# Kernel optimization log

Hardware: AMD Instinct MI355X
Metric: run time of the kernel (lower is better)

The kernel has to match this reference:

```python
import jax, jax.numpy as jnp
import numpy as np

N = 100000
D = 128
E = 1600000
NUM_STEPS = 8
LAM0 = 1.0
LAM1 = 1.0
ALPHA = 1.0 / (1.0 + 0.0 + LAM0 + LAM1)  # args.alp == 0 path


def setup_inputs() -> dict:
    key = jax.random.key(0)
    ks = jax.random.split(key, 12)
    X = jax.random.normal(ks[0], (N, D), dtype=jnp.float32)
    # H init: normal(0, 1/in_features) + I  (notresidual=False branch)
    H1 = jax.random.normal(ks[1], (D, D), dtype=jnp.float32) * (1.0 / D) + jnp.eye(D, dtype=jnp.float32)
    H2 = jax.random.normal(ks[2], (D, D), dtype=jnp.float32) * (1.0 / D) + jnp.eye(D, dtype=jnp.float32)
    w_beta = jax.random.uniform(ks[3], (E,), dtype=jnp.float32)
    w_gamma = jax.random.uniform(ks[4], (E,), dtype=jnp.float32)
    d_beta = jax.random.uniform(ks[5], (N,), dtype=jnp.float32)
    d_gamma = jax.random.uniform(ks[6], (N,), dtype=jnp.float32)
    src_beta = jax.random.randint(ks[7], (E,), 0, N, dtype=jnp.int32)
    dst_beta = jax.random.randint(ks[8], (E,), 0, N, dtype=jnp.int32)
    src_gamma = jax.random.randint(ks[9], (E,), 0, N, dtype=jnp.int32)
    dst_gamma = jax.random.randint(ks[10], (E,), 0, N, dtype=jnp.int32)
    return {"X": X, "H1": H1, "H2": H2, "w_beta": w_beta, "w_gamma": w_gamma,
            "d_beta": d_beta, "d_gamma": d_gamma,
            "src_beta": src_beta, "dst_beta": dst_beta,
            "src_gamma": src_gamma, "dst_gamma": dst_gamma}


def _spmm(w, src, dst, Y):
    # (sparse A) @ Y with A[dst, src] = w
    return jax.ops.segment_sum(w[:, None] * Y[src], dst, num_segments=N)


def reference(X, H1, H2, w_beta, w_gamma, d_beta, d_gamma,
              src_beta, dst_beta, src_gamma, dst_gamma):
    # Q_tild = lam0*D_beta + lam1*D_gamma + I  (diagonal)
    q = LAM0 * d_beta + LAM1 * d_gamma + 1.0  # [N]
    S1 = H1 + H1.T
    P1 = H1 @ H1.T
    S2 = H2 + H2.T
    P2 = H2 @ H2.T
    Y0 = X
    Y = X
    for _ in range(NUM_STEPS):
        AbY = _spmm(w_beta, src_beta, dst_beta, Y)    # A_beta @ Y
        AgY = _spmm(w_gamma, src_gamma, dst_gamma, Y)  # A_gamma @ Y
        term_beta = AbY @ S1 - d_beta[:, None] * (Y @ P1)
        # L_gamma @ Y = D_gamma@Y - A_gamma@Y
        term_gamma = (d_gamma[:, None] * Y - AgY
                      + AgY @ S2 - d_gamma[:, None] * (Y @ P2))
        Y_hat = LAM0 * term_beta + Y0 + LAM1 * term_gamma
        Y = (1.0 - ALPHA) * Y + ALPHA * (Y_hat / q[:, None])
    return Y
```

## Files before the change

kernel.cpp:

```cpp
#include <hip/hip_runtime.h>
#include <cstdint>
#include <cstddef>

#define DD 128
#define ATS 68
#define ARS 132
#define BQS 132


__global__ void count2_k(const int* __restrict__ dstb, const int* __restrict__ dstg,
                         int* __restrict__ degb, int* __restrict__ degg, int E, int gE) {
    int b = blockIdx.x;
    const int* dst = (b < gE) ? dstb : dstg;
    int* deg = (b < gE) ? degb : degg;
    int i = ((b < gE) ? b : b - gE) * blockDim.x + threadIdx.x;
    if (i < E) atomicAdd(&deg[dst[i]], 1);
}

__global__ __launch_bounds__(1024) void scan2_k(const int* __restrict__ degb,
                                                const int* __restrict__ degg,
                                                int* __restrict__ rpb, int* __restrict__ rpg,
                                                int* __restrict__ curb, int* __restrict__ curg,
                                                int n) {
    const int* deg = (blockIdx.x == 0) ? degb : degg;
    int* rp = (blockIdx.x == 0) ? rpb : rpg;
    int* cur = (blockIdx.x == 0) ? curb : curg;
    __shared__ int sums[1024];
    int tid = threadIdx.x;
    int per = (n + 1023) >> 10;
    int start = tid * per;
    int end = min(start + per, n);
    int s = 0;
    for (int i = start; i < end; ++i) s += deg[i];
    sums[tid] = s;
    __syncthreads();
    for (int off = 1; off < 1024; off <<= 1) {
        int v = (tid >= off) ? sums[tid - off] : 0;
        __syncthreads();
        sums[tid] += v;
        __syncthreads();
    }
    int pre = (tid == 0) ? 0 : sums[tid - 1];
    for (int i = start; i < end; ++i) {
        rp[i] = pre;
        cur[i] = pre;
        pre += deg[i];
    }
    if (end == n) rp[n] = pre;
}

__global__ void fill2_k(const int* __restrict__ srcb, const int* __restrict__ dstb,
                        const float* __restrict__ wb,
                        const int* __restrict__ srcg, const int* __restrict__ dstg,
                        const float* __restrict__ wg,
                        int* __restrict__ curb, int* __restrict__ curg,
                        int2* __restrict__ eb, int2* __restrict__ eg, int E, int gE) {
    int b = blockIdx.x;
    bool isb = (b < gE);
    const int* src = isb ? srcb : srcg;
    const int* dst = isb ? dstb : dstg;
    const float* w = isb ? wb : wg;
    int* cur = isb ? curb : curg;
    int2* edges = isb ? eb : eg;
    int i = (isb ? b : b - gE) * blockDim.x + threadIdx.x;
    if (i < E) {
        int d = dst[i];
        int pos = atomicAdd(&cur[d], 1);
        edges[pos] = make_int2(src[i], __float_as_int(w[i]));
    }
}


__global__ __launch_bounds__(256) void prep_k(const float* __restrict__ H,
                                              float* __restrict__ P,
                                              float* __restrict__ S) {
    int idx = blockIdx.x * 256 + threadIdx.x;
    int i = idx >> 7, j = idx & 127;
    float acc = 0.f;
    for (int k = 0; k < DD; ++k) acc += H[i * DD + k] * H[j * DD + k];
    P[idx] = acc;
    S[idx] = H[i * DD + j] + H[j * DD + i];
}


__global__ __launch_bounds__(256, 3) void step_k(
    const float* __restrict__ Yc, const float* __restrict__ X,
    const int* __restrict__ rpb, const int2* __restrict__ eb,
    const int* __restrict__ rpg, const int2* __restrict__ eg,
    const float* __restrict__ db, const float* __restrict__ dg,
    const float* __restrict__ P1, const float* __restrict__ P2,
    const float* __restrict__ S1, const float* __restrict__ S2,
    float* __restrict__ Yn, int n)
{
    __shared__ float At[DD * ATS];
    __shared__ float U[32 * ARS];

    const int tid = threadIdx.x;
    const int lane = tid & 63;
    const int wv = tid >> 6;
    const int cg = tid & 15;
    const int rg = tid >> 4;
    const int row0 = blockIdx.x * 64;

    float aS[4][8], aP1[4][8], aP2[4][8];
#pragma unroll
    for (int i = 0; i < 4; ++i)
#pragma unroll
        for (int j = 0; j < 8; ++j) { aS[i][j] = 0.f; aP1[i][j] = 0.f; aP2[i][j] = 0.f; }

    auto gatherA = [&](const int* __restrict__ rp, const int2* __restrict__ edges) {
        for (int h = 0; h < 2; ++h) {
#pragma unroll 1
            for (int it = 0; it < 8; ++it) {
                int r = wv * 8 + it;
                int node = row0 + h * 32 + r;
                float a0 = 0.f, a1 = 0.f;
                if (node < n) {
                    int beg = rp[node], end = rp[node + 1];
                    int j = beg;
                    for (; j + 4 <= end; j += 4) {
                        int2 e0 = edges[j + 0], e1 = edges[j + 1];
                        int2 e2 = edges[j + 2], e3 = edges[j + 3];
                        float2 f0 = *((const float2*)(Yc + (size_t)e0.x * DD) + lane);
                        float2 f1 = *((const float2*)(Yc + (size_t)e1.x * DD) + lane);
                        float2 f2 = *((const float2*)(Yc + (size_t)e2.x * DD) + lane);
                        float2 f3 = *((const float2*)(Yc + (size_t)e3.x * DD) + lane);
                        float w0 = __int_as_float(e0.y), w1 = __int_as_float(e1.y);
                        float w2 = __int_as_float(e2.y), w3 = __int_as_float(e3.y);
                        a0 += w0 * f0.x; a1 += w0 * f0.y;
                        a0 += w1 * f1.x; a1 += w1 * f1.y;
                        a0 += w2 * f2.x; a1 += w2 * f2.y;
                        a0 += w3 * f3.x; a1 += w3 * f3.y;
                    }
                    for (; j < end; ++j) {
                        int2 e = edges[j];
                        float2 f = *((const float2*)(Yc + (size_t)e.x * DD) + lane);
                        float wv2 = __int_as_float(e.y);
                        a0 += wv2 * f.x; a1 += wv2 * f.y;
                    }
                }
                *reinterpret_cast<float2*>(&U[r * ARS + 2 * lane]) = make_float2(a0, a1);
            }
            __syncthreads();
            {
                int r = tid & 31;
                int cb = (tid >> 5) * 16;
#pragma unroll
                for (int u = 0; u < 4; ++u) {
                    float4 v = *reinterpret_cast<const float4*>(&U[r * ARS + cb + 4 * u]);
                    int c = cb + 4 * u;
                    At[(c + 0) * ATS + h * 32 + r] = v.x;
                    At[(c + 1) * ATS + h * 32 + r] = v.y;
                    At[(c + 2) * ATS + h * 32 + r] = v.z;
                    At[(c + 3) * ATS + h * 32 + r] = v.w;
                }
            }
            __syncthreads();
        }
    };

    auto stageY = [&]() {
        int r = tid >> 2;
        int rowc = min(row0 + r, n - 1);
        const float* gp = Yc + (size_t)rowc * DD;
#pragma unroll
        for (int i = 0; i < 8; ++i) {
            int c = ((tid & 3) << 2) + (i << 4);
            float4 v = *reinterpret_cast<const float4*>(gp + c);
            At[(c + 0) * ATS + r] = v.x;
            At[(c + 1) * ATS + r] = v.y;
            At[(c + 2) * ATS + r] = v.z;
            At[(c + 3) * ATS + r] = v.w;
        }
    };

    auto gemm = [&](const float* __restrict__ M, float (&acc)[4][8]) {
#pragma unroll 1
        for (int kq = 0; kq < 4; ++kq) {
            {
                int kl = tid & 31;
                int cb = (tid >> 5) * 16;
                const float* gp = M + (size_t)(kq * 32 + kl) * DD + cb;
                float* bp = U + kl * BQS + cb;
#pragma unroll
                for (int u = 0; u < 4; ++u)
                    *reinterpret_cast<float4*>(bp + 4 * u) =
                        *reinterpret_cast<const float4*>(gp + 4 * u);
            }
            __syncthreads();
#pragma unroll 2
            for (int kl = 0; kl < 32; ++kl) {
                int k = kq * 32 + kl;
                float4 a = *reinterpret_cast<const float4*>(&At[k * ATS + rg * 4]);
                float4 b0 = *reinterpret_cast<const float4*>(&U[kl * BQS + cg * 4]);
                float4 b1 = *reinterpret_cast<const float4*>(&U[kl * BQS + 64 + cg * 4]);
                float av[4] = {a.x, a.y, a.z, a.w};
                float bv[8] = {b0.x, b0.y, b0.z, b0.w, b1.x, b1.y, b1.z, b1.w};
#pragma unroll
                for (int i = 0; i < 4; ++i)
#pragma unroll
                    for (int j = 0; j < 8; ++j) acc[i][j] += av[i] * bv[j];
            }
            __syncthreads();
        }
    };

    gatherA(rpb, eb);
    gemm(S1, aS);

    gatherA(rpg, eg);
    gemm(S2, aS);
#pragma unroll
    for (int i = 0; i < 4; ++i) {
        int r = rg * 4 + i;
#pragma unroll
        for (int j = 0; j < 8; ++j) {
            int c = (j >> 2) * 64 + cg * 4 + (j & 3);
            aS[i][j] -= At[c * ATS + r];
        }
    }
    __syncthreads();

    stageY();
    __syncthreads();
    gemm(P1, aP1);
    gemm(P2, aP2);

    const float AL = 1.0f / 3.0f;
#pragma unroll
    for (int i = 0; i < 4; ++i) {
        int row = row0 + rg * 4 + i;
        if (row < n) {
            float dbv = db[row], dgv = dg[row];
            float aq = AL / (dbv + dgv + 1.0f);
#pragma unroll
            for (int hh = 0; hh < 2; ++hh) {
                size_t off = (size_t)row * DD + hh * 64 + cg * 4;
                float4 y = *reinterpret_cast<const float4*>(Yc + off);
                float4 x = *reinterpret_cast<const float4*>(X + off);
                float yv[4] = {y.x, y.y, y.z, y.w};
                float xv[4] = {x.x, x.y, x.z, x.w};
                float ov[4];
#pragma unroll
                for (int q = 0; q < 4; ++q) {
                    int j = hh * 4 + q;
                    float yhat = aS[i][j] - dbv * aP1[i][j] - dgv * aP2[i][j]
                                 + xv[q] + dgv * yv[q];
                    ov[q] = (1.0f - AL) * yv[q] + yhat * aq;
                }
                *reinterpret_cast<float4*>(Yn + off) = make_float4(ov[0], ov[1], ov[2], ov[3]);
            }
        }
    }
}


extern "C" void kernel_launch(void* const* d_in, const int* in_sizes, int n_in,
                              void* d_out, int out_size, void* d_ws, size_t ws_size,
                              hipStream_t stream) {
    const float* X   = (const float*)d_in[0];
    const float* H1  = (const float*)d_in[1];
    const float* H2  = (const float*)d_in[2];
    const float* wb  = (const float*)d_in[3];
    const float* wg  = (const float*)d_in[4];
    const float* db  = (const float*)d_in[5];
    const float* dg  = (const float*)d_in[6];
    const int* srcb  = (const int*)d_in[7];
    const int* dstb  = (const int*)d_in[8];
    const int* srcg  = (const int*)d_in[9];
    const int* dstg  = (const int*)d_in[10];
    const int N = in_sizes[5];
    const int E = in_sizes[3];
    float* Yout = (float*)d_out;

    char* p = (char*)d_ws;
    auto alloc = [&](size_t b) -> void* {
        void* r = (void*)p;
        p += (b + 255) & ~(size_t)255;
        return r;
    };
    float* P1 = (float*)alloc((size_t)DD * DD * 4);
    float* S1 = (float*)alloc((size_t)DD * DD * 4);
    float* P2 = (float*)alloc((size_t)DD * DD * 4);
    float* S2 = (float*)alloc((size_t)DD * DD * 4);
    int* degb = (int*)alloc((size_t)N * 4);
    int* degg = (int*)alloc((size_t)N * 4);
    int* rpb  = (int*)alloc((size_t)(N + 1) * 4);
    int* rpg  = (int*)alloc((size_t)(N + 1) * 4);
    int* curb = (int*)alloc((size_t)N * 4);
    int* curg = (int*)alloc((size_t)N * 4);
    int2* eb  = (int2*)alloc((size_t)E * 8);
    int2* eg  = (int2*)alloc((size_t)E * 8);
    float* Yw  = (float*)alloc((size_t)N * DD * 4);

    hipMemsetAsync(degb, 0, (size_t)N * 4, stream);
    hipMemsetAsync(degg, 0, (size_t)N * 4, stream);

    int gE = (E + 255) / 256;
    count2_k<<<2 * gE, 256, 0, stream>>>(dstb, dstg, degb, degg, E, gE);
    scan2_k<<<2, 1024, 0, stream>>>(degb, degg, rpb, rpg, curb, curg, N);
    fill2_k<<<2 * gE, 256, 0, stream>>>(srcb, dstb, wb, srcg, dstg, wg,
                                        curb, curg, eb, eg, E, gE);
    prep_k<<<64, 256, 0, stream>>>(H1, P1, S1);
    prep_k<<<64, 256, 0, stream>>>(H2, P2, S2);

    const float* Ycur = X;
    float* Ybufs[2] = {Yw, Yout};
    int gd = (N + 63) / 64;
    for (int s = 0; s < 8; ++s) {
        float* Yn = Ybufs[s & 1];
        step_k<<<gd, 256, 0, stream>>>(Ycur, X, rpb, eb, rpg, eg, db, dg,
                                       P1, P2, S1, S2, Yn, N);
        Ycur = Yn;
    }
}
```

Before: 4.771 ms.

## Split step into gather+P-gemm mixed kernel and separate S-gemm kernel

Each iteration's fused kernel is split in two. The first launch interleaves gather-only blocks (one node per wavefront, 8-way unrolled edge loop) with P1/P2 GEMM blocks, and writes AbY, AgY and a residual R to global memory. The second kernel stages those buffers, applies S1/S2, and combines everything into Y. This is meant to decouple latency-bound gathers from the GEMM and stop the per-block syncs inside the gather phase, at the cost of extra global traffic for three N×D intermediates and a second launch per step.

```diff
diff --git a/kernel.cpp b/kernel.cpp
--- a/kernel.cpp
+++ b/kernel.cpp
@@ -4,7 +4,6 @@
 
 #define DD 128
 #define ATS 68
-#define ARS 132
 #define BQS 132
 
 
@@ -83,83 +82,99 @@
 }
 
 
-__global__ __launch_bounds__(256, 3) void step_k(
+__device__ __forceinline__ void gather_row(const int* __restrict__ rp,
+                                           const int2* __restrict__ edges,
+                                           const float* __restrict__ Y,
+                                           float* __restrict__ out,
+                                           int node, int lane) {
+    int beg = rp[node], end = rp[node + 1];
+    float a0 = 0.f, a1 = 0.f;
+    int j = beg;
+    for (; j + 8 <= end; j += 8) {
+        int2 e0 = edges[j + 0], e1 = edges[j + 1], e2 = edges[j + 2], e3 = edges[j + 3];
+        int2 e4 = edges[j + 4], e5 = edges[j + 5], e6 = edges[j + 6], e7 = edges[j + 7];
+        float2 f0 = *((const float2*)(Y + (size_t)e0.x * DD) + lane);
+        float2 f1 = *((const float2*)(Y + (size_t)e1.x * DD) + lane);
+        float2 f2 = *((const float2*)(Y + (size_t)e2.x * DD) + lane);
+        float2 f3 = *((const float2*)(Y + (size_t)e3.x * DD) + lane);
+        float2 f4 = *((const float2*)(Y + (size_t)e4.x * DD) + lane);
+        float2 f5 = *((const float2*)(Y + (size_t)e5.x * DD) + lane);
+        float2 f6 = *((const float2*)(Y + (size_t)e6.x * DD) + lane);
+        float2 f7 = *((const float2*)(Y + (size_t)e7.x * DD) + lane);
+        float w0 = __int_as_float(e0.y), w1 = __int_as_float(e1.y);
+        float w2 = __int_as_float(e2.y), w3 = __int_as_float(e3.y);
+        float w4 = __int_as_float(e4.y), w5 = __int_as_float(e5.y);
+        float w6 = __int_as_float(e6.y), w7 = __int_as_float(e7.y);
+        a0 += w0 * f0.x; a1 += w0 * f0.y;
+        a0 += w1 * f1.x; a1 += w1 * f1.y;
+        a0 += w2 * f2.x; a1 += w2 * f2.y;
+        a0 += w3 * f3.x; a1 += w3 * f3.y;
+        a0 += w4 * f4.x; a1 += w4 * f4.y;
+        a0 += w5 * f5.x; a1 += w5 * f5.y;
+        a0 += w6 * f6.x; a1 += w6 * f6.y;
+        a0 += w7 * f7.x; a1 += w7 * f7.y;
+    }
+    for (; j + 4 <= end; j += 4) {
+        int2 e0 = edges[j + 0], e1 = edges[j + 1], e2 = edges[j + 2], e3 = edges[j + 3];
+        float2 f0 = *((const float2*)(Y + (size_t)e0.x * DD) + lane);
+        float2 f1 = *((const float2*)(Y + (size_t)e1.x * DD) + lane);
+        float2 f2 = *((const float2*)(Y + (size_t)e2.x * DD) + lane);
+        float2 f3 = *((const float2*)(Y + (size_t)e3.x * DD) + lane);
+        float w0 = __int_as_float(e0.y), w1 = __int_as_float(e1.y);
+        float w2 = __int_as_float(e2.y), w3 = __int_as_float(e3.y);
+        a0 += w0 * f0.x; a1 += w0 * f0.y;
+        a0 += w1 * f1.x; a1 += w1 * f1.y;
+        a0 += w2 * f2.x; a1 += w2 * f2.y;
+        a0 += w3 * f3.x; a1 += w3 * f3.y;
+    }
+    for (; j < end; ++j) {
+        int2 e = edges[j];
+        float2 f = *((const float2*)(Y + (size_t)e.x * DD) + lane);
+        float wv = __int_as_float(e.y);
+        a0 += wv * f.x; a1 += wv * f.y;
+    }
+    *((float2*)(out + (size_t)node * DD) + lane) = make_float2(a0, a1);
+}
+
+
+__global__ __launch_bounds__(256, 3) void k1_mixed(
     const float* __restrict__ Yc, const float* __restrict__ X,
     const int* __restrict__ rpb, const int2* __restrict__ eb,
     const int* __restrict__ rpg, const int2* __restrict__ eg,
     const float* __restrict__ db, const float* __restrict__ dg,
     const float* __restrict__ P1, const float* __restrict__ P2,
-    const float* __restrict__ S1, const float* __restrict__ S2,
-    float* __restrict__ Yn, int n)
+    float* __restrict__ AbY, float* __restrict__ AgY,
+    float* __restrict__ R, int n, int nd)
 {
     __shared__ float At[DD * ATS];
-    __shared__ float U[32 * ARS];
-
+    __shared__ float U[32 * BQS];
+
+    const int bid = blockIdx.x;
     const int tid = threadIdx.x;
-    const int lane = tid & 63;
-    const int wv = tid >> 6;
+
+    if ((bid & 15) != 15) {
+        int sbid = bid - (bid >> 4);
+        int node = sbid * 4 + (tid >> 6);
+        if (node >= n) return;
+        int lane = tid & 63;
+        gather_row(rpb, eb, Yc, AbY, node, lane);
+        gather_row(rpg, eg, Yc, AgY, node, lane);
+        return;
+    }
+
+    int dbid = bid >> 4;
+    if (dbid >= nd) return;
     const int cg = tid & 15;
     const int rg = tid >> 4;
-    const int row0 = blockIdx.x * 64;
-
-    float aS[4][8], aP1[4][8], aP2[4][8];
+    const int row0 = dbid * 64;
+
+    float aP1[4][8], aP2[4][8];
 #pragma unroll
     for (int i = 0; i < 4; ++i)
 #pragma unroll
-        for (int j = 0; j < 8; ++j) { aS[i][j] = 0.f; aP1[i][j] = 0.f; aP2[i][j] = 0.f; }
-
-    auto gatherA = [&](const int* __restrict__ rp, const int2* __restrict__ edges) {
-        for (int h = 0; h < 2; ++h) {
-#pragma unroll 1
-            for (int it = 0; it < 8; ++it) {
-                int r = wv * 8 + it;
-                int node = row0 + h * 32 + r;
-                float a0 = 0.f, a1 = 0.f;
-                if (node < n) {
-                    int beg = rp[node], end = rp[node + 1];
-                    int j = beg;
-                    for (; j + 4 <= end; j += 4) {
-                        int2 e0 = edges[j + 0], e1 = edges[j + 1];
-                        int2 e2 = edges[j + 2], e3 = edges[j + 3];
-                        float2 f0 = *((const float2*)(Yc + (size_t)e0.x * DD) + lane);
-                        float2 f1 = *((const float2*)(Yc + (size_t)e1.x * DD) + lane);
-                        float2 f2 = *((const float2*)(Yc + (size_t)e2.x * DD) + lane);
-                        float2 f3 = *((const float2*)(Yc + (size_t)e3.x * DD) + lane);
-                        float w0 = __int_as_float(e0.y), w1 = __int_as_float(e1.y);
-                        float w2 = __int_as_float(e2.y), w3 = __int_as_float(e3.y);
-                        a0 += w0 * f0.x; a1 += w0 * f0.y;
-                        a0 += w1 * f1.x; a1 += w1 * f1.y;
-                        a0 += w2 * f2.x; a1 += w2 * f2.y;
-                        a0 += w3 * f3.x; a1 += w3 * f3.y;
-                    }
-                    for (; j < end; ++j) {
-                        int2 e = edges[j];
-                        float2 f = *((const float2*)(Yc + (size_t)e.x * DD) + lane);
-                        float wv2 = __int_as_float(e.y);
-                        a0 += wv2 * f.x; a1 += wv2 * f.y;
-                    }
-                }
-                *reinterpret_cast<float2*>(&U[r * ARS + 2 * lane]) = make_float2(a0, a1);
-            }
-            __syncthreads();
-            {
-                int r = tid & 31;
-                int cb = (tid >> 5) * 16;
-#pragma unroll
-                for (int u = 0; u < 4; ++u) {
-                    float4 v = *reinterpret_cast<const float4*>(&U[r * ARS + cb + 4 * u]);
-                    int c = cb + 4 * u;
-                    At[(c + 0) * ATS + h * 32 + r] = v.x;
-                    At[(c + 1) * ATS + h * 32 + r] = v.y;
-                    At[(c + 2) * ATS + h * 32 + r] = v.z;
-                    At[(c + 3) * ATS + h * 32 + r] = v.w;
-                }
-            }
-            __syncthreads();
-        }
-    };
-
-    auto stageY = [&]() {
+        for (int j = 0; j < 8; ++j) { aP1[i][j] = 0.f; aP2[i][j] = 0.f; }
+
+    {
         int r = tid >> 2;
         int rowc = min(row0 + r, n - 1);
         const float* gp = Yc + (size_t)rowc * DD;
@@ -172,7 +187,8 @@
             At[(c + 2) * ATS + r] = v.z;
             At[(c + 3) * ATS + r] = v.w;
         }
-    };
+    }
+    __syncthreads();
 
     auto gemm = [&](const float* __restrict__ M, float (&acc)[4][8]) {
 #pragma unroll 1
@@ -205,34 +221,14 @@
         }
     };
 
-    gatherA(rpb, eb);
-    gemm(S1, aS);
-
-    gatherA(rpg, eg);
-    gemm(S2, aS);
-#pragma unroll
-    for (int i = 0; i < 4; ++i) {
-        int r = rg * 4 + i;
-#pragma unroll
-        for (int j = 0; j < 8; ++j) {
-            int c = (j >> 2) * 64 + cg * 4 + (j & 3);
-            aS[i][j] -= At[c * ATS + r];
-        }
-    }
-    __syncthreads();
-
-    stageY();
-    __syncthreads();
     gemm(P1, aP1);
     gemm(P2, aP2);
 
-    const float AL = 1.0f / 3.0f;
 #pragma unroll
     for (int i = 0; i < 4; ++i) {
         int row = row0 + rg * 4 + i;
         if (row < n) {
             float dbv = db[row], dgv = dg[row];
-            float aq = AL / (dbv + dgv + 1.0f);
 #pragma unroll
             for (int hh = 0; hh < 2; ++hh) {
                 size_t off = (size_t)row * DD + hh * 64 + cg * 4;
@@ -244,9 +240,118 @@
 #pragma unroll
                 for (int q = 0; q < 4; ++q) {
                     int j = hh * 4 + q;
-                    float yhat = aS[i][j] - dbv * aP1[i][j] - dgv * aP2[i][j]
-                                 + xv[q] + dgv * yv[q];
-                    ov[q] = (1.0f - AL) * yv[q] + yhat * aq;
+                    ov[q] = xv[q] + dgv * yv[q] - dbv * aP1[i][j] - dgv * aP2[i][j];
+                }
+                *reinterpret_cast<float4*>(R + off) = make_float4(ov[0], ov[1], ov[2], ov[3]);
+            }
+        }
+    }
+}
+
+
+__global__ __launch_bounds__(256, 3) void k2_sgemm(
+    const float* __restrict__ Yc, const float* __restrict__ AbY,
+    const float* __restrict__ AgY, const float* __restrict__ R,
+    const float* __restrict__ db, const float* __restrict__ dg,
+    const float* __restrict__ S1, const float* __restrict__ S2,
+    float* __restrict__ Yn, int n)
+{
+    __shared__ float At[DD * ATS];
+    __shared__ float U[32 * BQS];
+
+    const int tid = threadIdx.x;
+    const int cg = tid & 15;
+    const int rg = tid >> 4;
+    const int row0 = blockIdx.x * 64;
+
+    float aS[4][8];
+#pragma unroll
+    for (int i = 0; i < 4; ++i)
+#pragma unroll
+        for (int j = 0; j < 8; ++j) aS[i][j] = 0.f;
+
+    auto stageT = [&](const float* __restrict__ G) {
+        int r = tid >> 2;
+        int rowc = min(row0 + r, n - 1);
+        const float* gp = G + (size_t)rowc * DD;
+#pragma unroll
+        for (int i = 0; i < 8; ++i) {
+            int c = ((tid & 3) << 2) + (i << 4);
+            float4 v = *reinterpret_cast<const float4*>(gp + c);
+            At[(c + 0) * ATS + r] = v.x;
+            At[(c + 1) * ATS + r] = v.y;
+            At[(c + 2) * ATS + r] = v.z;
+            At[(c + 3) * ATS + r] = v.w;
+        }
+    };
+    auto gemm = [&](const float* __restrict__ M, float (&acc)[4][8]) {
+#pragma unroll 1
+        for (int kq = 0; kq < 4; ++kq) {
+            {
+                int kl = tid & 31;
+                int cb = (tid >> 5) * 16;
+                const float* gp = M + (size_t)(kq * 32 + kl) * DD + cb;
+                float* bp = U + kl * BQS + cb;
+#pragma unroll
+                for (int u = 0; u < 4; ++u)
+                    *reinterpret_cast<float4*>(bp + 4 * u) =
+                        *reinterpret_cast<const float4*>(gp + 4 * u);
+            }
+            __syncthreads();
+#pragma unroll 2
+            for (int kl = 0; kl < 32; ++kl) {
+                int k = kq * 32 + kl;
+                float4 a = *reinterpret_cast<const float4*>(&At[k * ATS + rg * 4]);
+                float4 b0 = *reinterpret_cast<const float4*>(&U[kl * BQS + cg * 4]);
+                float4 b1 = *reinterpret_cast<const float4*>(&U[kl * BQS + 64 + cg * 4]);
+                float av[4] = {a.x, a.y, a.z, a.w};
+                float bv[8] = {b0.x, b0.y, b0.z, b0.w, b1.x, b1.y, b1.z, b1.w};
+#pragma unroll
+                for (int i = 0; i < 4; ++i)
+#pragma unroll
+                    for (int j = 0; j < 8; ++j) acc[i][j] += av[i] * bv[j];
+            }
+            __syncthreads();
+        }
+    };
+
+    stageT(AbY);
+    __syncthreads();
+    gemm(S1, aS);
+
+    stageT(AgY);
+    __syncthreads();
+    gemm(S2, aS);
+
+#pragma unroll
+    for (int i = 0; i < 4; ++i) {
+        int r = rg * 4 + i;
+#pragma unroll
+        for (int j = 0; j < 8; ++j) {
+            int c = (j >> 2) * 64 + cg * 4 + (j & 3);
+            aS[i][j] -= At[c * ATS + r];
+        }
+    }
+
+    const float AL = 1.0f / 3.0f;
+#pragma unroll
+    for (int i = 0; i < 4; ++i) {
+        int row = row0 + rg * 4 + i;
+        if (row < n) {
+            float dbv = db[row], dgv = dg[row];
+            float aq = AL / (dbv + dgv + 1.0f);
+#pragma unroll
+            for (int hh = 0; hh < 2; ++hh) {
+                size_t off = (size_t)row * DD + hh * 64 + cg * 4;
+                float4 y = *reinterpret_cast<const float4*>(Yc + off);
+                float4 rr = *reinterpret_cast<const float4*>(R + off);
+                float yv[4] = {y.x, y.y, y.z, y.w};
+                float rv[4] = {rr.x, rr.y, rr.z, rr.w};
+                float ov[4];
+#pragma unroll
+                for (int q = 0; q < 4; ++q) {
+                    int j = hh * 4 + q;
+                    ov[q] = (1.0f - AL) * yv[q] + (aS[i][j] + rv[q]) * aq;
                 }
                 *reinterpret_cast<float4*>(Yn + off) = make_float4(ov[0], ov[1], ov[2], ov[3]);
             }
@@ -291,6 +396,9 @@
     int* curg = (int*)alloc((size_t)N * 4);
     int2* eb  = (int2*)alloc((size_t)E * 8);
     int2* eg  = (int2*)alloc((size_t)E * 8);
+    float* AbY = (float*)alloc((size_t)N * DD * 4);
+    float* AgY = (float*)alloc((size_t)N * DD * 4);
+    float* Rt  = (float*)alloc((size_t)N * DD * 4);
     float* Yw  = (float*)alloc((size_t)N * DD * 4);
 
     hipMemsetAsync(degb, 0, (size_t)N * 4, stream);
@@ -307,10 +415,15 @@
     const float* Ycur = X;
     float* Ybufs[2] = {Yw, Yout};
     int gd = (N + 63) / 64;
+    int ns = (N + 3) / 4;
+    long long T = ((long long)ns * 16 + 14) / 15;
+    if (T / 16 < gd) T = (long long)gd * 16;
     for (int s = 0; s < 8; ++s) {
         float* Yn = Ybufs[s & 1];
-        step_k<<<gd, 256, 0, stream>>>(Ycur, X, rpb, eb, rpg, eg, db, dg,
-                                       P1, P2, S1, S2, Yn, N);
+        k1_mixed<<<(int)T, 256, 0, stream>>>(Ycur, X, rpb, eb, rpg, eg, db, dg,
+                                             P1, P2, AbY, AgY, Rt, N, gd);
+        k2_sgemm<<<gd, 256, 0, stream>>>(Ycur, AbY, AgY, Rt, db, dg,
+                                         S1, S2, Yn, N);
         Ycur = Yn;
     }
 }
```

New measurement: 9.718 ms. +103.7%, slower.

## Split fused step into a separate high-occupancy SpMM kernel and a dense GEMM kernel

Applied to the files above, without the earlier changes.

The fused per-step kernel, which gathered neighbors and ran the dense GEMMs at 3 blocks per CU, is split into two kernels. spmm2_k computes both A_beta@Y and A_gamma@Y for one node per wavefront at higher occupancy, interleaving the two edge lists to expose more memory parallelism. dense4_k then stages those results from global buffers and runs the small GEMMs. This aims to hide gather latency better, at the cost of writing and reading two extra N×128 intermediate arrays each step.

```diff
diff --git a/kernel.cpp b/kernel.cpp
--- a/kernel.cpp
+++ b/kernel.cpp
@@ -4,7 +4,6 @@
 
 #define DD 128
 #define ATS 68
-#define ARS 132
 #define BQS 132
 
 
@@ -83,21 +82,102 @@
 }
 
 
-__global__ __launch_bounds__(256, 3) void step_k(
-    const float* __restrict__ Yc, const float* __restrict__ X,
+__global__ __launch_bounds__(256, 8) void spmm2_k(
     const int* __restrict__ rpb, const int2* __restrict__ eb,
     const int* __restrict__ rpg, const int2* __restrict__ eg,
+    const float* __restrict__ Y,
+    float* __restrict__ outb, float* __restrict__ outg, int n)
+{
+    int node = blockIdx.x * 4 + (threadIdx.x >> 6);
+    if (node >= n) return;
+    int lane = threadIdx.x & 63;
+
+    int jb = rpb[node], be = rpb[node + 1];
+    int jg = rpg[node], ge = rpg[node + 1];
+    float b0 = 0.f, b1 = 0.f, g0 = 0.f, g1 = 0.f;
+
+    while (jb + 4 <= be && jg + 4 <= ge) {
+        int2 x0 = eb[jb + 0], x1 = eb[jb + 1], x2 = eb[jb + 2], x3 = eb[jb + 3];
+        int2 y0 = eg[jg + 0], y1 = eg[jg + 1], y2 = eg[jg + 2], y3 = eg[jg + 3];
+        float2 fb0 = *((const float2*)(Y + (size_t)x0.x * DD) + lane);
+        float2 fb1 = *((const float2*)(Y + (size_t)x1.x * DD) + lane);
+        float2 fb2 = *((const float2*)(Y + (size_t)x2.x * DD) + lane);
+        float2 fb3 = *((const float2*)(Y + (size_t)x3.x * DD) + lane);
+        float2 fg0 = *((const float2*)(Y + (size_t)y0.x * DD) + lane);
+        float2 fg1 = *((const float2*)(Y + (size_t)y1.x * DD) + lane);
+        float2 fg2 = *((const float2*)(Y + (size_t)y2.x * DD) + lane);
+        float2 fg3 = *((const float2*)(Y + (size_t)y3.x * DD) + lane);
+        float wb0 = __int_as_float(x0.y), wb1 = __int_as_float(x1.y);
+        float wb2 = __int_as_float(x2.y), wb3 = __int_as_float(x3.y);
+        float wg0 = __int_as_float(y0.y), wg1 = __int_as_float(y1.y);
+        float wg2 = __int_as_float(y2.y), wg3 = __int_as_float(y3.y);
+        b0 += wb0 * fb0.x; b1 += wb0 * fb0.y;
+        b0 += wb1 * fb1.x; b1 += wb1 * fb1.y;
+        b0 += wb2 * fb2.x; b1 += wb2 * fb2.y;
+        b0 += wb3 * fb3.x; b1 += wb3 * fb3.y;
+        g0 += wg0 * fg0.x; g1 += wg0 * fg0.y;
+        g0 += wg1 * fg1.x; g1 += wg1 * fg1.y;
+        g0 += wg2 * fg2.x; g1 += wg2 * fg2.y;
+        g0 += wg3 * fg3.x; g1 += wg3 * fg3.y;
+        jb += 4; jg += 4;
+    }
+    while (jb + 4 <= be) {
+        int2 x0 = eb[jb + 0], x1 = eb[jb + 1], x2 = eb[jb + 2], x3 = eb[jb + 3];
+        float2 f0 = *((const float2*)(Y + (size_t)x0.x * DD) + lane);
+        float2 f1 = *((const float2*)(Y + (size_t)x1.x * DD) + lane);
+        float2 f2 = *((const float2*)(Y + (size_t)x2.x * DD) + lane);
+        float2 f3 = *((const float2*)(Y + (size_t)x3.x * DD) + lane);
+        float w0 = __int_as_float(x0.y), w1 = __int_as_float(x1.y);
+        float w2 = __int_as_float(x2.y), w3 = __int_as_float(x3.y);
+        b0 += w0 * f0.x; b1 += w0 * f0.y;
+        b0 += w1 * f1.x; b1 += w1 * f1.y;
+        b0 += w2 * f2.x; b1 += w2 * f2.y;
+        b0 += w3 * f3.x; b1 += w3 * f3.y;
+        jb += 4;
+    }
+    while (jg + 4 <= ge) {
+        int2 y0 = eg[jg + 0], y1 = eg[jg + 1], y2 = eg[jg + 2], y3 = eg[jg + 3];
+        float2 f0 = *((const float2*)(Y + (size_t)y0.x * DD) + lane);
+        float2 f1 = *((const float2*)(Y + (size_t)y1.x * DD) + lane);
+        float2 f2 = *((const float2*)(Y + (size_t)y2.x * DD) + lane);
+        float2 f3 = *((const float2*)(Y + (size_t)y3.x * DD) + lane);
+        float w0 = __int_as_float(y0.y), w1 = __int_as_float(y1.y);
+        float w2 = __int_as_float(y2.y), w3 = __int_as_float(y3.y);
+        g0 += w0 * f0.x; g1 += w0 * f0.y;
+        g0 += w1 * f1.x; g1 += w1 * f1.y;
+        g0 += w2 * f2.x; g1 += w2 * f2.y;
+        g0 += w3 * f3.x; g1 += w3 * f3.y;
+        jg += 4;
+    }
+    for (; jb < be; ++jb) {
+        int2 e = eb[jb];
+        float2 f = *((const float2*)(Y + (size_t)e.x * DD) + lane);
+        float wv = __int_as_float(e.y);
+        b0 += wv * f.x; b1 += wv * f.y;
+    }
+    for (; jg < ge; ++jg) {
+        int2 e = eg[jg];
+        float2 f = *((const float2*)(Y + (size_t)e.x * DD) + lane);
+        float wv = __int_as_float(e.y);
+        g0 += wv * f.x; g1 += wv * f.y;
+    }
+    *((float2*)(outb + (size_t)node * DD) + lane) = make_float2(b0, b1);
+    *((float2*)(outg + (size_t)node * DD) + lane) = make_float2(g0, g1);
+}
+
+
+__global__ __launch_bounds__(256, 3) void dense4_k(
+    const float* __restrict__ Yc, const float* __restrict__ X,
+    const float* __restrict__ AbY, const float* __restrict__ AgY,
     const float* __restrict__ db, const float* __restrict__ dg,
     const float* __restrict__ P1, const float* __restrict__ P2,
     const float* __restrict__ S1, const float* __restrict__ S2,
     float* __restrict__ Yn, int n)
 {
     __shared__ float At[DD * ATS];
-    __shared__ float U[32 * ARS];
+    __shared__ float U[32 * BQS];
 
     const int tid = threadIdx.x;
-    const int lane = tid & 63;
-    const int wv = tid >> 6;
     const int cg = tid & 15;
     const int rg = tid >> 4;
     const int row0 = blockIdx.x * 64;
@@ -108,61 +188,10 @@
 #pragma unroll
         for (int j = 0; j < 8; ++j) { aS[i][j] = 0.f; aP1[i][j] = 0.f; aP2[i][j] = 0.f; }
 
-    auto gatherA = [&](const int* __restrict__ rp, const int2* __restrict__ edges) {
-        for (int h = 0; h < 2; ++h) {
-#pragma unroll 1
-            for (int it = 0; it < 8; ++it) {
-                int r = wv * 8 + it;
-                int node = row0 + h * 32 + r;
-                float a0 = 0.f, a1 = 0.f;
-                if (node < n) {
-                    int beg = rp[node], end = rp[node + 1];
-                    int j = beg;
-                    for (; j + 4 <= end; j += 4) {
-                        int2 e0 = edges[j + 0], e1 = edges[j + 1];
-                        int2 e2 = edges[j + 2], e3 = edges[j + 3];
-                        float2 f0 = *((const float2*)(Yc + (size_t)e0.x * DD) + lane);
-                        float2 f1 = *((const float2*)(Yc + (size_t)e1.x * DD) + lane);
-                        float2 f2 = *((const float2*)(Yc + (size_t)e2.x * DD) + lane);
-                        float2 f3 = *((const float2*)(Yc + (size_t)e3.x * DD) + lane);
-                        float w0 = __int_as_float(e0.y), w1 = __int_as_float(e1.y);
-                        float w2 = __int_as_float(e2.y), w3 = __int_as_float(e3.y);
-                        a0 += w0 * f0.x; a1 += w0 * f0.y;
-                        a0 += w1 * f1.x; a1 += w1 * f1.y;
-                        a0 += w2 * f2.x; a1 += w2 * f2.y;
-                        a0 += w3 * f3.x; a1 += w3 * f3.y;
-                    }
-                    for (; j < end; ++j) {
-                        int2 e = edges[j];
-                        float2 f = *((const float2*)(Yc + (size_t)e.x * DD) + lane);
-                        float wv2 = __int_as_float(e.y);
-                        a0 += wv2 * f.x; a1 += wv2 * f.y;
-                    }
-                }
-                *reinterpret_cast<float2*>(&U[r * ARS + 2 * lane]) = make_float2(a0, a1);
-            }
-            __syncthreads();
-            {
-                int r = tid & 31;
-                int cb = (tid >> 5) * 16;
-#pragma unroll
-                for (int u = 0; u < 4; ++u) {
-                    float4 v = *reinterpret_cast<const float4*>(&U[r * ARS + cb + 4 * u]);
-                    int c = cb + 4 * u;
-                    At[(c + 0) * ATS + h * 32 + r] = v.x;
-                    At[(c + 1) * ATS + h * 32 + r] = v.y;
-                    At[(c + 2) * ATS + h * 32 + r] = v.z;
-                    At[(c + 3) * ATS + h * 32 + r] = v.w;
-                }
-            }
-            __syncthreads();
-        }
-    };
-
-    auto stageY = [&]() {
+    auto stageT = [&](const float* __restrict__ G) {
         int r = tid >> 2;
         int rowc = min(row0 + r, n - 1);
-        const float* gp = Yc + (size_t)rowc * DD;
+        const float* gp = G + (size_t)rowc * DD;
 #pragma unroll
         for (int i = 0; i < 8; ++i) {
             int c = ((tid & 3) << 2) + (i << 4);
@@ -173,7 +202,6 @@
             At[(c + 3) * ATS + r] = v.w;
         }
     };
-
     auto gemm = [&](const float* __restrict__ M, float (&acc)[4][8]) {
 #pragma unroll 1
         for (int kq = 0; kq < 4; ++kq) {
@@ -205,10 +233,12 @@
         }
     };
 
-    gatherA(rpb, eb);
+    stageT(AbY);
+    __syncthreads();
     gemm(S1, aS);
 
-    gatherA(rpg, eg);
+    stageT(AgY);
+    __syncthreads();
     gemm(S2, aS);
 #pragma unroll
     for (int i = 0; i < 4; ++i) {
@@ -221,7 +251,7 @@
     }
     __syncthreads();
 
-    stageY();
+    stageT(Yc);
     __syncthreads();
     gemm(P1, aP1);
     gemm(P2, aP2);
@@ -244,8 +274,8 @@
 #pragma unroll
                 for (int q = 0; q < 4; ++q) {
                     int j = hh * 4 + q;
-                    float yhat = aS[i][j] - dbv * aP1[i][j] - dgv * aP2[i][j]
-                                 + xv[q] + dgv * yv[q];
+                    float yhat = aS[i][j] + xv[q] + dgv * yv[q]
+                                 - dbv * aP1[i][j] - dgv * aP2[i][j];
                     ov[q] = (1.0f - AL) * yv[q] + yhat * aq;
                 }
                 *reinterpret_cast<float4*>(Yn + off) = make_float4(ov[0], ov[1], ov[2], ov[3]);
@@ -291,6 +321,8 @@
     int* curg = (int*)alloc((size_t)N * 4);
     int2* eb  = (int2*)alloc((size_t)E * 8);
     int2* eg  = (int2*)alloc((size_t)E * 8);
+    float* AbY = (float*)alloc((size_t)N * DD * 4);
+    float* AgY = (float*)alloc((size_t)N * DD * 4);
     float* Yw  = (float*)alloc((size_t)N * DD * 4);
 
     hipMemsetAsync(degb, 0, (size_t)N * 4, stream);
@@ -306,11 +338,13 @@
 
     const float* Ycur = X;
     float* Ybufs[2] = {Yw, Yout};
+    int gs = (N + 3) / 4;
     int gd = (N + 63) / 64;
     for (int s = 0; s < 8; ++s) {
         float* Yn = Ybufs[s & 1];
-        step_k<<<gd, 256, 0, stream>>>(Ycur, X, rpb, eb, rpg, eg, db, dg,
-                                       P1, P2, S1, S2, Yn, N);
+        spmm2_k<<<gs, 256, 0, stream>>>(rpb, eb, rpg, eg, Ycur, AbY, AgY, N);
+        dense4_k<<<gd, 256, 0, stream>>>(Ycur, X, AbY, AgY, db, dg,
+                                         P1, P2, S1, S2, Yn, N);
         Ycur = Yn;
     }
 }
```

Result: faster. 3.955 ms (-17.1%).
